# Kernel tuning notes

Hardware: AMD Instinct MI355X
Metric: run time of the kernel (lower is better)

Reference implementation:

```python
import jax, jax.numpy as jnp
import numpy as np


def gcn_conv(x, edge_index, W, b):
    """PyG-style GCNConv: add self-loops, symmetric degree norm, scatter-add."""
    N = x.shape[0]
    loops = jnp.arange(N, dtype=edge_index.dtype)
    src = jnp.concatenate([edge_index[0], loops])  # message sources
    dst = jnp.concatenate([edge_index[1], loops])  # aggregation targets
    h = x @ W  # [N, out] linear transform before propagation
    deg = jax.ops.segment_sum(jnp.ones_like(dst, dtype=h.dtype), dst, num_segments=N)
    dinv = jnp.where(deg > 0, jax.lax.rsqrt(jnp.maximum(deg, 1.0)), 0.0)
    norm = dinv[src] * dinv[dst]  # [E+N]
    msgs = norm[:, None] * h[src]  # gather + scale
    out = jax.ops.segment_sum(msgs, dst, num_segments=N)  # scatter-add
    return out + b


def setup_inputs() -> dict:
    key = jax.random.key(0)
    k1, k2, k3, k4 = jax.random.split(key, 4)
    N, E, F, H, C = 100000, 3200000, 256, 32, 16
    x = jax.random.normal(k1, (N, F), dtype=jnp.float32)
    edge_index = jax.random.randint(k2, (2, E), 0, N)
    W1 = jax.random.normal(k3, (F, H), dtype=jnp.float32) * 0.05
    b1 = jnp.zeros((H,), dtype=jnp.float32)
    W2 = jax.random.normal(k4, (H, C), dtype=jnp.float32) * 0.1
    b2 = jnp.zeros((C,), dtype=jnp.float32)
    return {"x": x, "edge_index": edge_index, "W1": W1, "b1": b1, "W2": W2, "b2": b2}


def reference(x, edge_index, W1, b1, W2, b2):
    h = jax.nn.relu(gcn_conv(x, edge_index, W1, b1))
    out = gcn_conv(h, edge_index, W2, b2)
    return jax.nn.softmax(out, axis=1)
```

## Files before the change

kernel.cpp:

```cpp
#include <hip/hip_runtime.h>
#include <math.h>

constexpr int Fdim = 256;
constexpr int Hdim = 32;
constexpr int Cdim = 16;
constexpr int CAP = 88;
constexpr int EPB = 8192;
constexpr int MAXNB = 512;

__global__ __launch_bounds__(256) void k_zero_int(int* __restrict__ p, int n) {
  int i = blockIdx.x * blockDim.x + threadIdx.x;
  if (i < n) p[i] = 0;
}

__global__ __launch_bounds__(256) void k_binB(const int* __restrict__ src,
                                              const int* __restrict__ dst,
                                              int* __restrict__ bcur,
                                              unsigned* __restrict__ pairs,
                                              int e, int nb, int bcap) {
  __shared__ int hist[MAXNB];
  __shared__ int cbase[MAXNB];
  int lo = blockIdx.x * EPB;
  int hi = lo + EPB;
  if (hi > e) hi = e;
  for (int t = threadIdx.x; t < nb; t += 256) hist[t] = 0;
  __syncthreads();
  for (int i = lo + threadIdx.x; i < hi; i += 256) {
    atomicAdd(&hist[dst[i] >> 8], 1);
  }
  __syncthreads();
  for (int t = threadIdx.x; t < nb; t += 256) {
    int h = hist[t];
    int base = h ? atomicAdd(&bcur[t], h) : 0;
    cbase[t] = t * bcap + base;
    hist[t] = 0;
  }
  __syncthreads();
  for (int i = lo + threadIdx.x; i < hi; i += 256) {
    int d = dst[i];
    int bk = d >> 8;
    int o = atomicAdd(&hist[bk], 1);
    int idx = cbase[bk] + o;
    if (idx < (bk + 1) * bcap)
      pairs[idx] = ((unsigned)(d & 255) << 24) | (unsigned)src[i];
  }
}

__global__ __launch_bounds__(256) void k_binC(const int* __restrict__ bcur,
                                              const unsigned* __restrict__ pairs,
                                              int* __restrict__ csr,
                                              int* __restrict__ cntg,
                                              float* __restrict__ dinv,
                                              int n, int bcap) {
  __shared__ int cnt2[256];
  __shared__ int cur2[256];
  int b = blockIdx.x;
  int nE = bcur[b];
  if (nE > bcap) nE = bcap;
  int base = b * bcap;
  cnt2[threadIdx.x] = 0;
  __syncthreads();
  for (int i = threadIdx.x; i < nE; i += 256) {
    atomicAdd(&cnt2[pairs[base + i] >> 24], 1);
  }
  __syncthreads();
  int d = b * 256 + threadIdx.x;
  int c = cnt2[threadIdx.x];
  if (d < n) {
    cntg[d] = c;
    dinv[d] = 1.0f / sqrtf((float)(c + 1));
  }
  cur2[threadIdx.x] = 0;
  __syncthreads();
  for (int i = threadIdx.x; i < nE; i += 256) {
    unsigned w = pairs[base + i];
    int loc = (int)(w >> 24);
    int s = (int)(w & 0xFFFFFFu);
    int o = atomicAdd(&cur2[loc], 1);
    if (o < CAP) csr[(size_t)(b * 256 + loc) * CAP + o] = s;
  }
}

__global__ __launch_bounds__(256) void k_lin1(const float4* __restrict__ x4,
                                              const float* __restrict__ W,
                                              const float* __restrict__ dinv,
                                              float4* __restrict__ hs, int n) {
  int row = blockIdx.x * blockDim.x + threadIdx.x;
  if (row >= n) return;
  float acc[Hdim];
#pragma unroll
  for (int c = 0; c < Hdim; ++c) acc[c] = 0.f;
  const float4* xr = x4 + (size_t)row * (Fdim / 4);
#pragma unroll 1
  for (int k4 = 0; k4 < Fdim / 4; ++k4) {
    float4 xv = xr[k4];
    const float* wp = W + k4 * 4 * Hdim;
#pragma unroll
    for (int c = 0; c < Hdim; ++c) acc[c] = fmaf(xv.x, wp[c], acc[c]);
#pragma unroll
    for (int c = 0; c < Hdim; ++c) acc[c] = fmaf(xv.y, wp[Hdim + c], acc[c]);
#pragma unroll
    for (int c = 0; c < Hdim; ++c) acc[c] = fmaf(xv.z, wp[2 * Hdim + c], acc[c]);
#pragma unroll
    for (int c = 0; c < Hdim; ++c) acc[c] = fmaf(xv.w, wp[3 * Hdim + c], acc[c]);
  }
  float di = dinv[row];
  float4* hp = hs + (size_t)row * (Hdim / 4);
#pragma unroll
  for (int q = 0; q < Hdim / 4; ++q) {
    float4 v;
    v.x = di * acc[4 * q + 0];
    v.y = di * acc[4 * q + 1];
    v.z = di * acc[4 * q + 2];
    v.w = di * acc[4 * q + 3];
    hp[q] = v;
  }
}

__global__ __launch_bounds__(256) void k_g1l2(const int* __restrict__ cnt,
                                              const int* __restrict__ csr,
                                              const float4* __restrict__ hs,
                                              const float* __restrict__ dinv,
                                              const float* __restrict__ b1,
                                              const float* __restrict__ W2,
                                              float4* __restrict__ hs2, int n) {
  int t = blockIdx.x * blockDim.x + threadIdx.x;
  int d = t >> 3, f = t & 7;
  if (d >= n) return;
  int c = cnt[d];
  if (c > CAP) c = CAP;
  const int* row = csr + (size_t)d * CAP;
  float4 acc = hs[(size_t)d * 8 + f];
  int k = 0;
  for (; k + 1 < c; k += 2) {
    int s0 = row[k], s1 = row[k + 1];
    float4 v0 = hs[(size_t)s0 * 8 + f];
    float4 v1 = hs[(size_t)s1 * 8 + f];
    acc.x += v0.x + v1.x; acc.y += v0.y + v1.y;
    acc.z += v0.z + v1.z; acc.w += v0.w + v1.w;
  }
  if (k < c) {
    int s = row[k];
    float4 v = hs[(size_t)s * 8 + f];
    acc.x += v.x; acc.y += v.y; acc.z += v.z; acc.w += v.w;
  }
  float di = dinv[d];
  float h[4];
  h[0] = fmaxf(fmaf(di, acc.x, b1[4 * f + 0]), 0.f);
  h[1] = fmaxf(fmaf(di, acc.y, b1[4 * f + 1]), 0.f);
  h[2] = fmaxf(fmaf(di, acc.z, b1[4 * f + 2]), 0.f);
  h[3] = fmaxf(fmaf(di, acc.w, b1[4 * f + 3]), 0.f);
  float p[Cdim];
#pragma unroll
  for (int j = 0; j < Cdim; ++j) p[j] = 0.f;
#pragma unroll
  for (int r = 0; r < 4; ++r) {
    const float* w = W2 + (4 * f + r) * Cdim;
#pragma unroll
    for (int j = 0; j < Cdim; ++j) p[j] = fmaf(h[r], w[j], p[j]);
  }
#pragma unroll
  for (int m = 1; m < 8; m <<= 1) {
#pragma unroll
    for (int j = 0; j < Cdim; ++j) p[j] += __shfl_xor(p[j], m, 64);
  }
  if (f < 4) {
    float4 o;
    o.x = di * p[4 * f + 0];
    o.y = di * p[4 * f + 1];
    o.z = di * p[4 * f + 2];
    o.w = di * p[4 * f + 3];
    hs2[(size_t)d * 4 + f] = o;
  }
}

__global__ __launch_bounds__(256) void k_g2sm(const int* __restrict__ cnt,
                                              const int* __restrict__ csr,
                                              const float4* __restrict__ hs,
                                              const float* __restrict__ dinv,
                                              const float* __restrict__ b2,
                                              float4* __restrict__ out, int n) {
  int t = blockIdx.x * blockDim.x + threadIdx.x;
  int d = t >> 2, f = t & 3;
  if (d >= n) return;
  int c = cnt[d];
  if (c > CAP) c = CAP;
  const int* row = csr + (size_t)d * CAP;
  float4 acc = hs[(size_t)d * 4 + f];
  int k = 0;
  for (; k + 1 < c; k += 2) {
    int s0 = row[k], s1 = row[k + 1];
    float4 v0 = hs[(size_t)s0 * 4 + f];
    float4 v1 = hs[(size_t)s1 * 4 + f];
    acc.x += v0.x + v1.x; acc.y += v0.y + v1.y;
    acc.z += v0.z + v1.z; acc.w += v0.w + v1.w;
  }
  if (k < c) {
    int s = row[k];
    float4 v = hs[(size_t)s * 4 + f];
    acc.x += v.x; acc.y += v.y; acc.z += v.z; acc.w += v.w;
  }
  float di = dinv[d];
  float v0 = fmaf(di, acc.x, b2[4 * f + 0]);
  float v1 = fmaf(di, acc.y, b2[4 * f + 1]);
  float v2 = fmaf(di, acc.z, b2[4 * f + 2]);
  float v3 = fmaf(di, acc.w, b2[4 * f + 3]);
  float m = fmaxf(fmaxf(v0, v1), fmaxf(v2, v3));
  m = fmaxf(m, __shfl_xor(m, 1, 64));
  m = fmaxf(m, __shfl_xor(m, 2, 64));
  float e0 = expf(v0 - m), e1 = expf(v1 - m), e2 = expf(v2 - m), e3 = expf(v3 - m);
  float s = e0 + e1 + e2 + e3;
  s += __shfl_xor(s, 1, 64);
  s += __shfl_xor(s, 2, 64);
  float inv = 1.f / s;
  float4 o;
  o.x = e0 * inv; o.y = e1 * inv; o.z = e2 * inv; o.w = e3 * inv;
  out[(size_t)d * 4 + f] = o;
}

extern "C" void kernel_launch(void* const* d_in, const int* in_sizes, int n_in,
                              void* d_out, int out_size, void* d_ws, size_t ws_size,
                              hipStream_t stream) {
  const float* x = (const float*)d_in[0];
  const int* ei = (const int*)d_in[1];
  const float* W1 = (const float*)d_in[2];
  const float* b1 = (const float*)d_in[3];
  const float* W2 = (const float*)d_in[4];
  const float* b2 = (const float*)d_in[5];
  float* out = (float*)d_out;

  const int N = in_sizes[0] / Fdim;
  const int E = in_sizes[1] / 2;
  const int* srcp = ei;
  const int* dstp = ei + E;

  const int NB = (N + 255) >> 8;
  const int mean = (E + NB - 1) / NB;
  const int BCAP = mean + mean / 16 + 256;

  char* ws = (char*)d_ws;
  int* bcur = (int*)ws;        ws += (size_t)MAXNB * 4;
  float* dinv = (float*)ws;    ws += (size_t)N * 4;
  int* cntg = (int*)ws;        ws += (size_t)N * 4;
  int* csr = (int*)ws;         ws += (size_t)N * CAP * 4;
  char* region = ws;
  unsigned* pairs = (unsigned*)region;
  float* hs1 = (float*)region;
  float* hs2 = (float*)(region + (size_t)N * Hdim * 4);

  int nb_n = (N + 255) / 256;
  int nbB = (E + EPB - 1) / EPB;

  k_zero_int<<<(NB + 255) / 256, 256, 0, stream>>>(bcur, NB);
  k_binB<<<nbB, 256, 0, stream>>>(srcp, dstp, bcur, pairs, E, NB, BCAP);
  k_binC<<<NB, 256, 0, stream>>>(bcur, pairs, csr, cntg, dinv, N, BCAP);

  k_lin1<<<nb_n, 256, 0, stream>>>((const float4*)x, W1, dinv, (float4*)hs1, N);

  int nb_g1 = (N * 8 + 255) / 256;
  k_g1l2<<<nb_g1, 256, 0, stream>>>(cntg, csr, (const float4*)hs1, dinv, b1, W2,
                                    (float4*)hs2, N);

  int nb_g2 = (N * 4 + 255) / 256;
  k_g2sm<<<nb_g2, 256, 0, stream>>>(cntg, csr, (const float4*)hs2, dinv, b2,
                                    (float4*)out, N);
}
```

Before: 261.0 us.

## Stage x tiles through shared memory and split K across two thread halves in lin1

```diff
diff --git a/kernel.cpp b/kernel.cpp
--- a/kernel.cpp
+++ b/kernel.cpp
@@ -81,39 +81,70 @@
   }
 }
 
-__global__ __launch_bounds__(256) void k_lin1(const float4* __restrict__ x4,
+__global__ __launch_bounds__(512) void k_lin1(const float4* __restrict__ x4,
                                               const float* __restrict__ W,
                                               const float* __restrict__ dinv,
                                               float4* __restrict__ hs, int n) {
-  int row = blockIdx.x * blockDim.x + threadIdx.x;
-  if (row >= n) return;
+  __shared__ float4 smem4[2][8][256];
+  int tid = threadIdx.x;
+  int h = tid >> 8;
+  int u = tid & 255;
+  int r0 = blockIdx.x << 8;
+
   float acc[Hdim];
 #pragma unroll
   for (int c = 0; c < Hdim; ++c) acc[c] = 0.f;
-  const float4* xr = x4 + (size_t)row * (Fdim / 4);
+
 #pragma unroll 1
-  for (int k4 = 0; k4 < Fdim / 4; ++k4) {
-    float4 xv = xr[k4];
-    const float* wp = W + k4 * 4 * Hdim;
-#pragma unroll
-    for (int c = 0; c < Hdim; ++c) acc[c] = fmaf(xv.x, wp[c], acc[c]);
-#pragma unroll
-    for (int c = 0; c < Hdim; ++c) acc[c] = fmaf(xv.y, wp[Hdim + c], acc[c]);
-#pragma unroll
-    for (int c = 0; c < Hdim; ++c) acc[c] = fmaf(xv.z, wp[2 * Hdim + c], acc[c]);
-#pragma unroll
-    for (int c = 0; c < Hdim; ++c) acc[c] = fmaf(xv.w, wp[3 * Hdim + c], acc[c]);
-  }
-  float di = dinv[row];
-  float4* hp = hs + (size_t)row * (Hdim / 4);
-#pragma unroll
-  for (int q = 0; q < Hdim / 4; ++q) {
-    float4 v;
-    v.x = di * acc[4 * q + 0];
-    v.y = di * acc[4 * q + 1];
-    v.z = di * acc[4 * q + 2];
-    v.w = di * acc[4 * q + 3];
-    hp[q] = v;
+  for (int cch = 0; cch < 4; ++cch) {
+    int colbase = h * 32 + cch * 8;
+#pragma unroll
+    for (int j = 0; j < 8; ++j) {
+      int idx = j * 256 + u;
+      int ri = idx >> 3, c4 = idx & 7;
+      int rr = r0 + ri;
+      if (rr >= n) rr = n - 1;
+      smem4[h][c4][ri] = x4[(size_t)rr * (Fdim / 4) + colbase + c4];
+    }
+    __syncthreads();
+#pragma unroll
+    for (int i = 0; i < 8; ++i) {
+      float4 xv = smem4[h][i][u];
+      const float* wp = W + (colbase + i) * 4 * Hdim;
+#pragma unroll
+      for (int c = 0; c < Hdim; ++c) acc[c] = fmaf(xv.x, wp[c], acc[c]);
+#pragma unroll
+      for (int c = 0; c < Hdim; ++c) acc[c] = fmaf(xv.y, wp[Hdim + c], acc[c]);
+#pragma unroll
+      for (int c = 0; c < Hdim; ++c) acc[c] = fmaf(xv.z, wp[2 * Hdim + c], acc[c]);
+#pragma unroll
+      for (int c = 0; c < Hdim; ++c) acc[c] = fmaf(xv.w, wp[3 * Hdim + c], acc[c]);
+    }
+    __syncthreads();
+  }
+
+  float* red = (float*)smem4;
+  if (h == 1) {
+#pragma unroll
+    for (int i = 0; i < 8; ++i) {
+      float4 v;
+      v.x = acc[4 * i + 0]; v.y = acc[4 * i + 1];
+      v.z = acc[4 * i + 2]; v.w = acc[4 * i + 3];
+      *(float4*)&red[u * 36 + 4 * i] = v;
+    }
+  }
+  __syncthreads();
+  if (h == 0 && r0 + u < n) {
+    float di = dinv[r0 + u];
+#pragma unroll
+    for (int i = 0; i < 8; ++i) {
+      float4 o = *(float4*)&red[u * 36 + 4 * i];
+      o.x = di * (o.x + acc[4 * i + 0]);
+      o.y = di * (o.y + acc[4 * i + 1]);
+      o.z = di * (o.z + acc[4 * i + 2]);
+      o.w = di * (o.w + acc[4 * i + 3]);
+      hs[(size_t)(r0 + u) * (Hdim / 4) + i] = o;
+    }
   }
 }
 
@@ -239,10 +270,10 @@
   const int BCAP = mean + mean / 16 + 256;
 
   char* ws = (char*)d_ws;
-  int* bcur = (int*)ws;        ws += (size_t)MAXNB * 4;
-  float* dinv = (float*)ws;    ws += (size_t)N * 4;
-  int* cntg = (int*)ws;        ws += (size_t)N * 4;
-  int* csr = (int*)ws;         ws += (size_t)N * CAP * 4;
+  int* bcur = (int*)ws;      ws += (size_t)MAXNB * 4;
+  float* dinv = (float*)ws;  ws += (size_t)N * 4;
+  int* cntg = (int*)ws;      ws += (size_t)N * 4;
+  int* csr = (int*)ws;       ws += (size_t)N * CAP * 4;
   char* region = ws;
   unsigned* pairs = (unsigned*)region;
   float* hs1 = (float*)region;
@@ -255,7 +286,7 @@
   k_binB<<<nbB, 256, 0, stream>>>(srcp, dstp, bcur, pairs, E, NB, BCAP);
   k_binC<<<NB, 256, 0, stream>>>(bcur, pairs, csr, cntg, dinv, N, BCAP);
 
-  k_lin1<<<nb_n, 256, 0, stream>>>((const float4*)x, W1, dinv, (float4*)hs1, N);
+  k_lin1<<<nb_n, 512, 0, stream>>>((const float4*)x, W1, dinv, (float4*)hs1, N);
 
   int nb_g1 = (N * 8 + 255) / 256;
   k_g1l2<<<nb_g1, 256, 0, stream>>>(cntg, csr, (const float4*)hs1, dinv, b1, W2,
```

After: 349.1 us. 33.8% more time.
